# Performance work log

Measured on AMD Instinct MI355X. Metric: run time of the kernel, lower is better.

The kernel has to match this reference:

```python
import jax, jax.numpy as jnp
import numpy as np

BATCH, INPUT_DIM, BOND_DIM, OUTPUT_DIM = 4096, 1024, 32, 512


def setup_inputs() -> dict:
    key = jax.random.key(0)
    k1, k2, k3 = jax.random.split(key, 3)
    # inputs centered at 1 so the length-1024 chain product stays O(1) in fp32
    inputs = 1.0 + 0.05 * jax.random.normal(k1, (BATCH, INPUT_DIM), dtype=jnp.float32)
    # cores scaled ~ glorot so each [bond,bond] step roughly preserves norm
    cores = jax.random.normal(k2, (INPUT_DIM, BOND_DIM, BOND_DIM), dtype=jnp.float32) / jnp.sqrt(jnp.float32(BOND_DIM))
    projection = jax.random.normal(k3, (BOND_DIM, OUTPUT_DIM), dtype=jnp.float32) * 0.05
    bias = jnp.zeros((OUTPUT_DIM,), dtype=jnp.float32)
    return {"inputs": inputs, "cores": cores, "projection": projection, "bias": bias}


def reference(inputs, cores, projection, bias):
    # MPS chain: boundary_{i+1}[b,k] = sum_j boundary_i[b,j] * x_i[b] * core_i[j,k]
    batch = inputs.shape[0]
    bond = cores.shape[1]
    boundary0 = jnp.ones((batch, bond), dtype=inputs.dtype)

    def step(boundary, xc):
        x_i, core_i = xc  # x_i: [batch], core_i: [bond, bond]
        new_boundary = (boundary * x_i[:, None]) @ core_i  # [batch, bond]
        return new_boundary, None

    xs = (inputs.T, cores)  # scan over input_dim axis
    final_boundary, _ = jax.lax.scan(step, boundary0, xs)
    return final_boundary @ projection + bias
```

## Files before the change

### kernel.cpp

```cpp
#include <hip/hip_runtime.h>


__device__ __forceinline__ void mm32(const float* __restrict__ A,
                                     const float* __restrict__ B,
                                     float* __restrict__ C, int tid) {
    const int j = tid >> 3;
    const int kq = tid & 7;
    float a[32];
    const float4* __restrict__ A4 = (const float4*)(A + j * 32);
#pragma unroll
    for (int t = 0; t < 8; ++t) {
        float4 v = A4[t];
        a[4 * t + 0] = v.x; a[4 * t + 1] = v.y;
        a[4 * t + 2] = v.z; a[4 * t + 3] = v.w;
    }
    const float4* __restrict__ B4 = (const float4*)B;
    float4 acc0 = make_float4(0.f, 0.f, 0.f, 0.f);
    float4 acc1 = make_float4(0.f, 0.f, 0.f, 0.f);
#pragma unroll
    for (int m = 0; m < 16; ++m) {
        float4 b0 = B4[m * 8 + kq];
        float4 b1 = B4[(m + 16) * 8 + kq];
        acc0.x = fmaf(a[m], b0.x, acc0.x);
        acc0.y = fmaf(a[m], b0.y, acc0.y);
        acc0.z = fmaf(a[m], b0.z, acc0.z);
        acc0.w = fmaf(a[m], b0.w, acc0.w);
        acc1.x = fmaf(a[m + 16], b1.x, acc1.x);
        acc1.y = fmaf(a[m + 16], b1.y, acc1.y);
        acc1.z = fmaf(a[m + 16], b1.z, acc1.z);
        acc1.w = fmaf(a[m + 16], b1.w, acc1.w);
    }
    float4 acc;
    acc.x = acc0.x + acc1.x; acc.y = acc0.y + acc1.y;
    acc.z = acc0.z + acc1.z; acc.w = acc0.w + acc1.w;
    ((float4*)(C + j * 32))[kq] = acc;
}

__global__ __launch_bounds__(256) void k1(const float* __restrict__ cores,
                                          const float* __restrict__ inputs,
                                          float* __restrict__ l1,
                                          float* __restrict__ p) {
    __shared__ __align__(16) float c[4 * 1024];
    __shared__ __align__(16) float ping[1024];
    __shared__ __align__(16) float pong[1024];
    const int tid = threadIdx.x;
    const int s = blockIdx.x;
    const int lane = tid & 63;
    const int wid = tid >> 6;

    const float4* src = (const float4*)(cores + (size_t)s * 4096);
    float4* cd = (float4*)c;
#pragma unroll
    for (int t = 0; t < 4; ++t) cd[tid + 256 * t] = src[tid + 256 * t];

    float prs[4];
#pragma unroll
    for (int rr = 0; rr < 4; ++rr) {
        const int row = s * 16 + wid * 4 + rr;
        const float4* in4 = (const float4*)(inputs + (size_t)row * 1024);
        float4 x0 = in4[lane];
        float4 x1 = in4[lane + 64];
        float4 x2 = in4[lane + 128];
        float4 x3 = in4[lane + 192];
        prs[rr] = ((x0.x * x0.y) * (x0.z * x0.w)) * ((x1.x * x1.y) * (x1.z * x1.w)) *
                  ((x2.x * x2.y) * (x2.z * x2.w)) * ((x3.x * x3.y) * (x3.z * x3.w));
    }
#pragma unroll
    for (int rr = 0; rr < 4; ++rr) {
        float pr = prs[rr];
#pragma unroll
        for (int msk = 1; msk < 64; msk <<= 1) pr *= __shfl_xor(pr, msk);
        if (lane == 0) p[s * 16 + wid * 4 + rr] = pr;
    }

    __syncthreads();
    mm32(c, c + 1024, ping, tid);
    __syncthreads();
    mm32(ping, c + 2048, pong, tid);
    __syncthreads();
    mm32(pong, c + 3072, ping, tid);
    __syncthreads();
    ((float4*)(l1 + (size_t)s * 1024))[tid] = ((const float4*)ping)[tid];
}

__global__ __launch_bounds__(256) void k2(const float* __restrict__ l1,
                                          float* __restrict__ l2) {
    __shared__ __align__(16) float m[16 * 1024];
    __shared__ __align__(16) float ping[1024];
    __shared__ __align__(16) float pong[1024];
    const int tid = threadIdx.x;
    const int s = blockIdx.x;
    const float4* src = (const float4*)(l1 + (size_t)s * 16384);
    float4* md = (float4*)m;
#pragma unroll
    for (int t = 0; t < 16; ++t) md[tid + 256 * t] = src[tid + 256 * t];
    __syncthreads();
    mm32(m, m + 1024, ping, tid);
    __syncthreads();
    float* A = ping;
    float* C = pong;
    for (int t = 2; t < 16; ++t) {
        mm32(A, m + t * 1024, C, tid);
        __syncthreads();
        float* tmp = A; A = C; C = tmp;
    }
    ((float4*)(l2 + (size_t)s * 1024))[tid] = ((const float4*)A)[tid];
}

__global__ __launch_bounds__(256) void k4(const float* __restrict__ l2,
                                          const float* __restrict__ proj,
                                          const float* __restrict__ p,
                                          const float* __restrict__ bias,
                                          float* __restrict__ out) {
    __shared__ __align__(16) float M[16 * 1024];
    __shared__ __align__(16) float qL[512];
    __shared__ __align__(16) float bL[512];
    __shared__ float pL[16];
    __shared__ float w[32];
    const int tid = threadIdx.x;
    const int s = blockIdx.x;

    const float4* src = (const float4*)l2;
    float4* Md = (float4*)M;
#pragma unroll
    for (int t = 0; t < 16; ++t) Md[tid + 256 * t] = src[tid + 256 * t];
    if (tid < 128) ((float4*)bL)[tid] = ((const float4*)bias)[tid];
    if (tid < 16) pL[tid] = p[s * 16 + tid];
    __syncthreads();

    if (tid < 64) {
        const int k = tid & 31;
        float v = 1.0f;
        for (int sm = 0; sm < 16; ++sm) {
            const float* mat = M + sm * 1024 + k;
            float a0 = 0.f, a1 = 0.f, a2 = 0.f, a3 = 0.f;
#pragma unroll
            for (int j = 0; j < 8; ++j) {
                a0 = fmaf(__shfl(v, j),      mat[32 * j],        a0);
                a1 = fmaf(__shfl(v, j + 8),  mat[32 * (j + 8)],  a1);
                a2 = fmaf(__shfl(v, j + 16), mat[32 * (j + 16)], a2);
                a3 = fmaf(__shfl(v, j + 24), mat[32 * (j + 24)], a3);
            }
            v = (a0 + a1) + (a2 + a3);
        }
        if (tid < 32) w[k] = v;
    }
    __syncthreads();

    if (tid < 128) {
        const float4* P4 = (const float4*)proj;
        float4 acc = make_float4(0.f, 0.f, 0.f, 0.f);
#pragma unroll
        for (int j = 0; j < 32; ++j) {
            float wj = w[j];
            float4 pv = P4[j * 128 + tid];
            acc.x = fmaf(wj, pv.x, acc.x);
            acc.y = fmaf(wj, pv.y, acc.y);
            acc.z = fmaf(wj, pv.z, acc.z);
            acc.w = fmaf(wj, pv.w, acc.w);
        }
        ((float4*)qL)[tid] = acc;
    }
    __syncthreads();

    const float4* q4 = (const float4*)qL;
    const float4* b4 = (const float4*)bL;
#pragma unroll
    for (int rb = 0; rb < 2; ++rb) {
        const int r8 = rb * 8 + (tid >> 5);
        const int row = s * 16 + r8;
        const float pr = pL[r8];
        float4* o4 = (float4*)(out + (size_t)row * 512);
#pragma unroll
        for (int u = 0; u < 4; ++u) {
            const int c4 = u * 32 + (tid & 31);
            float4 qq = q4[c4];
            float4 bb = b4[c4];
            float4 r;
            r.x = fmaf(pr, qq.x, bb.x);
            r.y = fmaf(pr, qq.y, bb.y);
            r.z = fmaf(pr, qq.z, bb.z);
            r.w = fmaf(pr, qq.w, bb.w);
            o4[c4] = r;
        }
    }
}

extern "C" void kernel_launch(void* const* d_in, const int* in_sizes, int n_in,
                              void* d_out, int out_size, void* d_ws, size_t ws_size,
                              hipStream_t stream) {
    const float* inputs = (const float*)d_in[0];
    const float* cores  = (const float*)d_in[1];
    const float* proj   = (const float*)d_in[2];
    const float* bias   = (const float*)d_in[3];
    float* out = (float*)d_out;
    float* w  = (float*)d_ws;
    float* l1 = w;
    float* l2 = w + 256 * 1024;
    float* p  = w + 256 * 1024 + 16 * 1024;

    k1<<<256, 256, 0, stream>>>(cores, inputs, l1, p);
    k2<<<16, 256, 0, stream>>>(l1, l2);
    k4<<<256, 256, 0, stream>>>(l2, proj, p, bias, out);
}
```

Measured before the change: 93.27 us.

## Fuse chain-reduction kernel into final kernel using atomic flag handoff

Merges the 16-block k2 reduction into the 256-block output kernel. The first 16 blocks compute the partial chain products and signal completion through a global atomic counter, and every block spins on that counter before reading l2. This removes one kernel launch and its launch gap. In exchange it relies on all 256 blocks being co-resident (or on the producer blocks being scheduled first), and the waiting blocks spin on the counter.

```diff
diff --git a/kernel.cpp b/kernel.cpp
--- a/kernel.cpp
+++ b/kernel.cpp
@@ -39,7 +39,8 @@
 __global__ __launch_bounds__(256) void k1(const float* __restrict__ cores,
                                           const float* __restrict__ inputs,
                                           float* __restrict__ l1,
-                                          float* __restrict__ p) {
+                                          float* __restrict__ p,
+                                          int* __restrict__ flag) {
     __shared__ __align__(16) float c[4 * 1024];
     __shared__ __align__(16) float ping[1024];
     __shared__ __align__(16) float pong[1024];
@@ -47,6 +48,8 @@
     const int s = blockIdx.x;
     const int lane = tid & 63;
     const int wid = tid >> 6;
+
+    if (s == 0 && tid == 0) *flag = 0;
 
     const float4* src = (const float4*)(cores + (size_t)s * 4096);
     float4* cd = (float4*)c;
@@ -83,36 +86,16 @@
     ((float4*)(l1 + (size_t)s * 1024))[tid] = ((const float4*)ping)[tid];
 }
 
-__global__ __launch_bounds__(256) void k2(const float* __restrict__ l1,
-                                          float* __restrict__ l2) {
-    __shared__ __align__(16) float m[16 * 1024];
+__global__ __launch_bounds__(256) void k4f(const float* __restrict__ l1,
+                                           float* __restrict__ l2,
+                                           int* __restrict__ flag,
+                                           const float* __restrict__ proj,
+                                           const float* __restrict__ p,
+                                           const float* __restrict__ bias,
+                                           float* __restrict__ out) {
+    __shared__ __align__(16) float M[16 * 1024];
     __shared__ __align__(16) float ping[1024];
     __shared__ __align__(16) float pong[1024];
-    const int tid = threadIdx.x;
-    const int s = blockIdx.x;
-    const float4* src = (const float4*)(l1 + (size_t)s * 16384);
-    float4* md = (float4*)m;
-#pragma unroll
-    for (int t = 0; t < 16; ++t) md[tid + 256 * t] = src[tid + 256 * t];
-    __syncthreads();
-    mm32(m, m + 1024, ping, tid);
-    __syncthreads();
-    float* A = ping;
-    float* C = pong;
-    for (int t = 2; t < 16; ++t) {
-        mm32(A, m + t * 1024, C, tid);
-        __syncthreads();
-        float* tmp = A; A = C; C = tmp;
-    }
-    ((float4*)(l2 + (size_t)s * 1024))[tid] = ((const float4*)A)[tid];
-}
-
-__global__ __launch_bounds__(256) void k4(const float* __restrict__ l2,
-                                          const float* __restrict__ proj,
-                                          const float* __restrict__ p,
-                                          const float* __restrict__ bias,
-                                          float* __restrict__ out) {
-    __shared__ __align__(16) float M[16 * 1024];
     __shared__ __align__(16) float qL[512];
     __shared__ __align__(16) float bL[512];
     __shared__ float pL[16];
@@ -120,12 +103,44 @@
     const int tid = threadIdx.x;
     const int s = blockIdx.x;
 
+    if (s < 16) {
+        const float4* srcP = (const float4*)(l1 + (size_t)s * 16384);
+        float4* Md = (float4*)M;
+#pragma unroll
+        for (int t = 0; t < 16; ++t) Md[tid + 256 * t] = srcP[tid + 256 * t];
+        __syncthreads();
+        mm32(M, M + 1024, ping, tid);
+        __syncthreads();
+        float* A = ping;
+        float* C = pong;
+        for (int t = 2; t < 16; ++t) {
+            mm32(A, M + t * 1024, C, tid);
+            __syncthreads();
+            float* tmp = A; A = C; C = tmp;
+        }
+        ((float4*)(l2 + (size_t)s * 1024))[tid] = ((const float4*)A)[tid];
+        __threadfence();
+        __syncthreads();
+        if (tid == 0)
+            __hip_atomic_fetch_add(flag, 1, __ATOMIC_RELEASE,
+                                   __HIP_MEMORY_SCOPE_AGENT);
+    }
+
+    if (tid < 128) ((float4*)bL)[tid] = ((const float4*)bias)[tid];
+    if (tid < 16) pL[tid] = p[s * 16 + tid];
+
+    if (tid == 0) {
+        while (__hip_atomic_load(flag, __ATOMIC_ACQUIRE,
+                                 __HIP_MEMORY_SCOPE_AGENT) < 16)
+            __builtin_amdgcn_s_sleep(2);
+    }
+    __syncthreads();
+    __threadfence();
+
     const float4* src = (const float4*)l2;
     float4* Md = (float4*)M;
 #pragma unroll
     for (int t = 0; t < 16; ++t) Md[tid + 256 * t] = src[tid + 256 * t];
-    if (tid < 128) ((float4*)bL)[tid] = ((const float4*)bias)[tid];
-    if (tid < 16) pL[tid] = p[s * 16 + tid];
     __syncthreads();
 
     if (tid < 64) {
@@ -194,12 +209,12 @@
     const float* proj   = (const float*)d_in[2];
     const float* bias   = (const float*)d_in[3];
     float* out = (float*)d_out;
-    float* w  = (float*)d_ws;
-    float* l1 = w;
-    float* l2 = w + 256 * 1024;
-    float* p  = w + 256 * 1024 + 16 * 1024;
-
-    k1<<<256, 256, 0, stream>>>(cores, inputs, l1, p);
-    k2<<<16, 256, 0, stream>>>(l1, l2);
-    k4<<<256, 256, 0, stream>>>(l2, proj, p, bias, out);
-}
+    float* wsf = (float*)d_ws;
+    float* l1 = wsf;
+    float* l2 = wsf + 256 * 1024;
+    float* p  = wsf + 256 * 1024 + 16 * 1024;
+    int* flag = (int*)(wsf + 256 * 1024 + 16 * 1024 + 4096 + 64);
+
+    k1<<<256, 256, 0, stream>>>(cores, inputs, l1, p, flag);
+    k4f<<<256, 256, 0, stream>>>(l1, l2, flag, proj, p, bias, out);
+}
```

Result: slower. 125.8 us (+34.9%).
